# Optimization experiments

Measured on AMD Instinct MI355X. Metric: run time of the kernel, lower is better.

## Reference

```python
import jax, jax.numpy as jnp
import numpy as np

D_TEMP = 64   # temporal_dim (even)
H = 4         # num_heads
KQ = 128      # kq_dim = temporal_dim + sum(cat_dims)
LD = 128      # output_latent_dim == value_dim
NREF = 128    # num_ref_points
MINT, MAXT = 0.0, 1.0


def time_emb(t):
    # sinusoidal embedding, cont_model='sinusoidal', learn_emb=False
    # z[..., 0::2] = sin(48*t * div), z[..., 1::2] = cos(48*t * div)
    pos = 48.0 * t[..., None]
    div = jnp.exp(jnp.arange(0, D_TEMP, 2, dtype=jnp.float32) * (-np.log(10.0) / D_TEMP))
    ang = pos * div
    return jnp.stack([jnp.sin(ang), jnp.cos(ang)], axis=-1).reshape(*t.shape, D_TEMP)


def setup_inputs() -> dict:
    key = jax.random.key(0)
    ks = jax.random.split(key, 10)
    N, T = 4, 1024
    ts = jax.random.uniform(ks[0], (N, T), jnp.float32)
    ys0 = jax.random.randint(ks[1], (N, T), 0, 100)
    ys1 = jax.random.randint(ks[2], (N, T), 0, 50)
    x = jax.random.normal(ks[3], (N, T, LD), jnp.float32)
    s = lambda k, sh: jax.random.normal(k, sh, jnp.float32) * 0.02
    emb0 = s(ks[4], (101, 32))   # class_sizes[0]+1 rows; last row = null/query class
    emb1 = s(ks[5], (51, 32))
    Wq = s(ks[6], (KQ, H * KQ)); bq = jnp.zeros((H * KQ,), jnp.float32)
    Wk = s(ks[7], (KQ, H * KQ)); bk = jnp.zeros((H * KQ,), jnp.float32)
    Wo = s(ks[8], (H * LD, LD)); bo = jnp.zeros((LD,), jnp.float32)
    return dict(ts=ts, ys0=ys0, ys1=ys1, x=x, emb0=emb0, emb1=emb1,
                Wq=Wq, bq=bq, Wk=Wk, bk=bk, Wo=Wo, bo=bo)


def reference(ts, ys0, ys1, x, emb0, emb1, Wq, bq, Wk, bk, Wo, bo):
    N, T = ts.shape
    # keys: time embedding || class embeddings at observed times  [N,T,KQ]
    zys = jnp.concatenate([emb0[ys0], emb1[ys1]], axis=-1)
    k_in = jnp.concatenate([time_emb(ts), zys], axis=-1)
    # queries: time embedding of reference points || null-class embedding [N,NREF,KQ]
    ref = jnp.linspace(MINT, MAXT, NREF, dtype=jnp.float32)
    q_null = jnp.concatenate([emb0[100], emb1[50]])  # extra embedding row
    q_in = jnp.concatenate([time_emb(ref), jnp.broadcast_to(q_null, (NREF, q_null.shape[0]))], axis=-1)
    q_in = jnp.broadcast_to(q_in[None], (N, NREF, KQ))
    # multi-head attention (math identical to the broadcast/elementwise original)
    hq = (q_in @ Wq + bq).reshape(N, NREF, H, KQ)
    hk = (k_in @ Wk + bk).reshape(N, T, H, KQ)
    scores = jnp.einsum('bqhd,bkhd->bhqk', hq, hk) / np.sqrt(KQ)
    p = jax.nn.softmax(scores, axis=-1)
    # value shared across heads: sum_k p * v  == matmul
    out = jnp.einsum('bhqk,bkv->bqhv', p, x).reshape(N, NREF, H * LD)
    return out @ Wo + bo  # [N, NREF, LD]
```

## Files before the change

### kernel.cpp

```cpp
#include <hip/hip_runtime.h>
#include <hip/hip_bf16.h>

#define N_B   4
#define T_LEN 1024
#define NREF  128
#define H     4
#define KQ    128
#define LD    128
#define HKQ   512
#define HLD   512

typedef __attribute__((ext_vector_type(8))) short bf16x8;
typedef __attribute__((ext_vector_type(4))) float f32x4;

union V8 { __hip_bfloat16 h[8]; bf16x8 v; };
union V4 { __hip_bfloat16 h[4]; ushort4 u; };

__device__ __forceinline__ void sincos_pair(float t, int i, float* s, float* c) {
    float div = __expf(-(float)(2 * i) * (2.302585093f / 64.0f));
    __sincosf(48.0f * t * div, s, c);
}

__global__ __launch_bounds__(256) void pack_kernel(
    const float* __restrict__ ts, const int* __restrict__ ys0, const int* __restrict__ ys1,
    const float* __restrict__ x,
    const float* __restrict__ emb0, const float* __restrict__ emb1,
    const float* __restrict__ Wq, const float* __restrict__ bq,
    const float* __restrict__ Wk, const float* __restrict__ Wo,
    const float* __restrict__ bo,
    __hip_bfloat16* __restrict__ A, __hip_bfloat16* __restrict__ kin,
    __hip_bfloat16* __restrict__ xT, __hip_bfloat16* __restrict__ WoT,
    float* __restrict__ out)
{
    __shared__ __align__(16) unsigned char smem[49152];
    int job = blockIdx.x;
    int tid = threadIdx.x;

    if (job < 8) {
        __hip_bfloat16* buf0 = (__hip_bfloat16*)smem;
        __hip_bfloat16* wlds = (__hip_bfloat16*)(smem + 16384);
        int h = job >> 1, qbase = (job & 1) * 64;

        for (int u = 0; u < 4; ++u) {
            int slot = u * 256 + tid;
            int q = slot >> 4;
            int c0 = (slot & 15) * 8;
            V8 v;
            if (c0 < 64) {
                float t = (float)(qbase + q) / 127.0f;
                #pragma unroll
                for (int jj = 0; jj < 8; jj += 2) {
                    float s, c;
                    sincos_pair(t, (c0 + jj) >> 1, &s, &c);
                    v.h[jj] = __float2bfloat16(s);
                    v.h[jj + 1] = __float2bfloat16(c);
                }
            } else if (c0 < 96) {
                #pragma unroll
                for (int jj = 0; jj < 8; ++jj) v.h[jj] = __float2bfloat16(emb0[100 * 32 + (c0 - 64) + jj]);
            } else {
                #pragma unroll
                for (int jj = 0; jj < 8; ++jj) v.h[jj] = __float2bfloat16(emb1[50 * 32 + (c0 - 96) + jj]);
            }
            int idx = (q * 128 + c0) ^ ((q & 7) << 3);
            *(bf16x8*)&buf0[idx] = v.v;
        }
        for (int u = 0; u < 16; ++u) {
            int s = u * 256 + tid;
            int i = s >> 5;
            int d0 = (s & 31) * 4;
            float4 w = *(const float4*)&Wq[(size_t)i * HKQ + h * KQ + d0];
            float wv[4] = {w.x, w.y, w.z, w.w};
            #pragma unroll
            for (int jj = 0; jj < 4; ++jj) {
                int d = d0 + jj;
                wlds[(d * 128 + i) ^ ((d & 7) << 3)] = __float2bfloat16(wv[jj]);
            }
        }
        __syncthreads();

        int wave = tid >> 6, lane = tid & 63, lm = lane & 15, lg = lane >> 4;
        f32x4 acc[8];
        #pragma unroll
        for (int dt = 0; dt < 8; ++dt) acc[dt] = f32x4{0.f, 0.f, 0.f, 0.f};
        #pragma unroll
        for (int ks = 0; ks < 4; ++ks) {
            int q = wave * 16 + lm;
            bf16x8 af = *(bf16x8*)&buf0[(q * 128 + ks * 32 + 8 * lg) ^ ((q & 7) << 3)];
            #pragma unroll
            for (int dt = 0; dt < 8; ++dt) {
                int d = dt * 16 + lm;
                bf16x8 bfr = *(bf16x8*)&wlds[(d * 128 + ks * 32 + 8 * lg) ^ ((d & 7) << 3)];
                acc[dt] = __builtin_amdgcn_mfma_f32_16x16x32_bf16(af, bfr, acc[dt], 0, 0, 0);
            }
        }
        __syncthreads();
        #pragma unroll
        for (int dt = 0; dt < 8; ++dt) {
            int d = dt * 16 + lm;
            float bb = bq[h * KQ + d];
            #pragma unroll
            for (int r = 0; r < 4; ++r) {
                int q = wave * 16 + 4 * lg + r;
                buf0[(q * 128 + d) ^ ((q & 7) << 3)] = __float2bfloat16(acc[dt][r] + bb);
            }
        }
        for (int u = 0; u < 16; ++u) {
            int s = u * 256 + tid;
            int i = s >> 5;
            int d0 = (s & 31) * 4;
            float4 w = *(const float4*)&Wk[(size_t)i * HKQ + h * KQ + d0];
            V4 bv;
            bv.h[0] = __float2bfloat16(w.x); bv.h[1] = __float2bfloat16(w.y);
            bv.h[2] = __float2bfloat16(w.z); bv.h[3] = __float2bfloat16(w.w);
            *(ushort4*)&wlds[(i * 128 + d0) ^ ((i & 7) << 3)] = bv.u;
        }
        __syncthreads();
        f32x4 acc2[8];
        #pragma unroll
        for (int it = 0; it < 8; ++it) acc2[it] = f32x4{0.f, 0.f, 0.f, 0.f};
        #pragma unroll
        for (int ks = 0; ks < 4; ++ks) {
            int q = wave * 16 + lm;
            bf16x8 af = *(bf16x8*)&buf0[(q * 128 + ks * 32 + 8 * lg) ^ ((q & 7) << 3)];
            #pragma unroll
            for (int it = 0; it < 8; ++it) {
                int i2 = it * 16 + lm;
                bf16x8 bv = *(bf16x8*)&wlds[(i2 * 128 + ks * 32 + 8 * lg) ^ ((i2 & 7) << 3)];
                acc2[it] = __builtin_amdgcn_mfma_f32_16x16x32_bf16(af, bv, acc2[it], 0, 0, 0);
            }
        }
        #pragma unroll
        for (int it = 0; it < 8; ++it) {
            int i2 = it * 16 + lm;
            #pragma unroll
            for (int r = 0; r < 4; ++r) {
                int q = qbase + wave * 16 + 4 * lg + r;
                A[((size_t)h * NREF + q) * KQ + i2] = __float2bfloat16(acc2[it][r]);
            }
        }
    } else if (job < 72) {
        int row0 = (job - 8) * 64;
        for (int u = 0; u < 4; ++u) {
            int slot = u * 256 + tid;
            int r = slot >> 4;
            int c0 = (slot & 15) * 8;
            int bt = row0 + r;
            V8 v;
            if (c0 < 64) {
                float t = ts[bt];
                #pragma unroll
                for (int jj = 0; jj < 8; jj += 2) {
                    float s, c;
                    sincos_pair(t, (c0 + jj) >> 1, &s, &c);
                    v.h[jj] = __float2bfloat16(s);
                    v.h[jj + 1] = __float2bfloat16(c);
                }
            } else if (c0 < 96) {
                int y = ys0[bt];
                #pragma unroll
                for (int jj = 0; jj < 8; ++jj) v.h[jj] = __float2bfloat16(emb0[y * 32 + (c0 - 64) + jj]);
            } else {
                int y = ys1[bt];
                #pragma unroll
                for (int jj = 0; jj < 8; ++jj) v.h[jj] = __float2bfloat16(emb1[y * 32 + (c0 - 96) + jj]);
            }
            *(bf16x8*)&kin[(size_t)bt * KQ + c0] = v.v;
        }
    } else if (job < 136) {
        __hip_bfloat16 (*tile)[136] = (__hip_bfloat16(*)[136])smem;
        int jb = job - 72;
        int b = jb >> 4, t0 = (jb & 15) * 64;
        for (int e = tid; e < 64 * 32; e += 256) {
            int tt = e >> 5, v4 = e & 31;
            float4 xv = *(const float4*)&x[((size_t)(b * T_LEN + t0 + tt)) * LD + v4 * 4];
            tile[tt][v4 * 4 + 0] = __float2bfloat16(xv.x);
            tile[tt][v4 * 4 + 1] = __float2bfloat16(xv.y);
            tile[tt][v4 * 4 + 2] = __float2bfloat16(xv.z);
            tile[tt][v4 * 4 + 3] = __float2bfloat16(xv.w);
        }
        __syncthreads();
        int v = tid >> 1, th = (tid & 1) * 32;
        for (int i = 0; i < 32; i += 4) {
            ushort4 u;
            u.x = *(unsigned short*)&tile[th + i + 0][v];
            u.y = *(unsigned short*)&tile[th + i + 1][v];
            u.z = *(unsigned short*)&tile[th + i + 2][v];
            u.w = *(unsigned short*)&tile[th + i + 3][v];
            *(ushort4*)&xT[((size_t)b * LD + v) * T_LEN + t0 + th + i] = u;
        }
    } else if (job < 144) {
        __hip_bfloat16 (*tile)[130] = (__hip_bfloat16(*)[130])smem;
        int i0 = (job - 136) * 64;
        for (int u = 0; u < 32; ++u) {
            int e = u * 256 + tid;
            int il = e >> 7, j = e & 127;
            tile[il][j] = __float2bfloat16(Wo[(size_t)(i0 + il) * LD + j]);
        }
        __syncthreads();
        for (int u = 0; u < 32; ++u) {
            int s = u * 256 + tid;
            int j = s >> 6, il = s & 63;
            WoT[(size_t)j * HLD + i0 + il] = tile[il][j];
        }
    } else {
        int b = job - 144;
        for (int e = tid; e < NREF * LD; e += 256)
            out[(size_t)b * NREF * LD + e] = bo[e & 127];
    }
}

__global__ __launch_bounds__(512) void attn_proj(const __hip_bfloat16* __restrict__ A,
                                                 const __hip_bfloat16* __restrict__ kin,
                                                 const __hip_bfloat16* __restrict__ xT,
                                                 const __hip_bfloat16* __restrict__ WoT,
                                                 float* __restrict__ out) {
    __shared__ __hip_bfloat16 P_lds[16 * 1024];
    __shared__ __hip_bfloat16 att_lds[16 * 128];
    __shared__ float redm[8][16], reds[8][16];

    int tid = threadIdx.x;
    int w = tid >> 6, lane = tid & 63;
    int lm = lane & 15, lg = lane >> 4;
    int q0 = blockIdx.x * 16, h = blockIdx.y, b = blockIdx.z;
    const float scale = 0.08838834764831845f;

    bf16x8 af[4];
    #pragma unroll
    for (int ks = 0; ks < 4; ++ks)
        af[ks] = *(const bf16x8*)(A + ((size_t)h * NREF + q0 + lm) * KQ + ks * 32 + lg * 8);

    f32x4 sacc[8];
    #pragma unroll
    for (int kt = 0; kt < 8; ++kt) sacc[kt] = f32x4{0.f, 0.f, 0.f, 0.f};
    #pragma unroll
    for (int ks = 0; ks < 4; ++ks) {
        #pragma unroll
        for (int kt = 0; kt < 8; ++kt) {
            bf16x8 bfr = *(const bf16x8*)(kin + (size_t)(b * T_LEN + w * 128 + kt * 16 + lm) * KQ + ks * 32 + lg * 8);
            sacc[kt] = __builtin_amdgcn_mfma_f32_16x16x32_bf16(af[ks], bfr, sacc[kt], 0, 0, 0);
        }
    }
    #pragma unroll
    for (int r = 0; r < 4; ++r) {
        float cm = sacc[0][r];
        #pragma unroll
        for (int kt = 1; kt < 8; ++kt) cm = fmaxf(cm, sacc[kt][r]);
        #pragma unroll
        for (int o = 8; o >= 1; o >>= 1) cm = fmaxf(cm, __shfl_xor(cm, o));
        if (lm == 0) redm[w][4 * lg + r] = cm;
    }
    __syncthreads();
    #pragma unroll
    for (int r = 0; r < 4; ++r) {
        int q = 4 * lg + r;
        float cm = redm[0][q];
        #pragma unroll
        for (int ww = 1; ww < 8; ++ww) cm = fmaxf(cm, redm[ww][q]);
        float fm = cm * scale;
        float sum = 0.f;
        #pragma unroll
        for (int kt = 0; kt < 8; ++kt) {
            float p = __expf(sacc[kt][r] * scale - fm);
            sum += p;
            int key = w * 128 + kt * 16 + lm;
            P_lds[(q * 1024 + key) ^ ((q & 7) << 3)] = __float2bfloat16(p);
        }
        #pragma unroll
        for (int o = 8; o >= 1; o >>= 1) sum += __shfl_xor(sum, o);
        if (lm == 0) reds[w][q] = sum;
    }
    __syncthreads();
    float l_[4];
    #pragma unroll
    for (int r = 0; r < 4; ++r) {
        int q = 4 * lg + r;
        float csum = reds[0][q];
        #pragma unroll
        for (int ww = 1; ww < 8; ++ww) csum += reds[ww][q];
        l_[r] = csum;
    }
    f32x4 oacc = f32x4{0.f, 0.f, 0.f, 0.f};
    const __hip_bfloat16* xb0 = xT + (size_t)(b * LD + w * 16 + lm) * T_LEN;
    #pragma unroll
    for (int ks2 = 0; ks2 < 32; ++ks2) {
        bf16x8 pa = *(bf16x8*)&P_lds[(lm * 1024 + ks2 * 32 + 8 * lg) ^ ((lm & 7) << 3)];
        bf16x8 xb = *(const bf16x8*)(xb0 + ks2 * 32 + lg * 8);
        oacc = __builtin_amdgcn_mfma_f32_16x16x32_bf16(pa, xb, oacc, 0, 0, 0);
    }
    #pragma unroll
    for (int r = 0; r < 4; ++r) {
        int q = 4 * lg + r;
        att_lds[(q * 128 + w * 16 + lm) ^ ((q & 7) << 3)] = __float2bfloat16(oacc[r] / l_[r]);
    }
    __syncthreads();
    f32x4 cacc = f32x4{0.f, 0.f, 0.f, 0.f};
    #pragma unroll
    for (int ks = 0; ks < 4; ++ks) {
        bf16x8 aa = *(bf16x8*)&att_lds[(lm * 128 + ks * 32 + 8 * lg) ^ ((lm & 7) << 3)];
        bf16x8 wb = *(const bf16x8*)(WoT + (size_t)(w * 16 + lm) * HLD + h * LD + ks * 32 + lg * 8);
        cacc = __builtin_amdgcn_mfma_f32_16x16x32_bf16(aa, wb, cacc, 0, 0, 0);
    }
    #pragma unroll
    for (int r = 0; r < 4; ++r) {
        int q = q0 + 4 * lg + r;
        atomicAdd(&out[((size_t)b * NREF + q) * LD + w * 16 + lm], cacc[r]);
    }
}

extern "C" void kernel_launch(void* const* d_in, const int* in_sizes, int n_in,
                              void* d_out, int out_size, void* d_ws, size_t ws_size,
                              hipStream_t stream) {
    const float* ts   = (const float*)d_in[0];
    const int*   ys0  = (const int*)d_in[1];
    const int*   ys1  = (const int*)d_in[2];
    const float* x    = (const float*)d_in[3];
    const float* emb0 = (const float*)d_in[4];
    const float* emb1 = (const float*)d_in[5];
    const float* Wq   = (const float*)d_in[6];
    const float* bq   = (const float*)d_in[7];
    const float* Wk   = (const float*)d_in[8];
    const float* Wo   = (const float*)d_in[10];
    const float* bo   = (const float*)d_in[11];
    float* out = (float*)d_out;

    __hip_bfloat16* bfws = (__hip_bfloat16*)d_ws;
    __hip_bfloat16* A   = bfws;
    __hip_bfloat16* kin = A + 65536;
    __hip_bfloat16* xT  = kin + 524288;
    __hip_bfloat16* WoT = xT + 524288;

    hipLaunchKernelGGL(pack_kernel, dim3(148), dim3(256), 0, stream,
                       ts, ys0, ys1, x, emb0, emb1, Wq, bq, Wk, Wo, bo, A, kin, xT, WoT, out);
    hipLaunchKernelGGL(attn_proj, dim3(8, 4, 4), dim3(512), 0, stream, A, kin, xT, WoT, out);
}
```

Measured before the change: 36.53 us.

## Fuse pack and attention kernels into one cooperative kernel with grid sync

Merges the packing kernel and the attention/projection kernel into a single cooperative launch of 128 blocks of 512 threads, separated by a grid-wide barrier. The packing jobs are re-partitioned onto 112 of the blocks at 512 threads each, which means fewer, larger blocks for the Q/K-projection prologue. This aims to remove the second kernel launch and the inter-kernel gap. In exchange it adds grid-sync overhead and cooperative-launch constraints, and the head-projection prologue now runs on only 4 blocks instead of 8, which lengthens that serial phase.

```diff
diff --git a/kernel.cpp b/kernel.cpp
--- a/kernel.cpp
+++ b/kernel.cpp
@@ -1,5 +1,8 @@
 #include <hip/hip_runtime.h>
 #include <hip/hip_bf16.h>
+#include <hip/hip_cooperative_groups.h>
+
+namespace cg = cooperative_groups;
 
 #define N_B   4
 #define T_LEN 1024
@@ -21,7 +24,7 @@
     __sincosf(48.0f * t * div, s, c);
 }
 
-__global__ __launch_bounds__(256) void pack_kernel(
+__global__ __launch_bounds__(512) void fused_all(
     const float* __restrict__ ts, const int* __restrict__ ys0, const int* __restrict__ ys1,
     const float* __restrict__ x,
     const float* __restrict__ emb0, const float* __restrict__ emb1,
@@ -32,22 +35,23 @@
     __hip_bfloat16* __restrict__ xT, __hip_bfloat16* __restrict__ WoT,
     float* __restrict__ out)
 {
-    __shared__ __align__(16) unsigned char smem[49152];
+    __shared__ __align__(16) unsigned char smem[65536];
+    int tid = threadIdx.x;
     int job = blockIdx.x;
-    int tid = threadIdx.x;
-
-    if (job < 8) {
+    const float scale = 0.08838834764831845f;
+
+    if (job < 4) {
         __hip_bfloat16* buf0 = (__hip_bfloat16*)smem;
-        __hip_bfloat16* wlds = (__hip_bfloat16*)(smem + 16384);
-        int h = job >> 1, qbase = (job & 1) * 64;
+        __hip_bfloat16* wlds = (__hip_bfloat16*)(smem + 32768);
+        int h = job;
 
         for (int u = 0; u < 4; ++u) {
-            int slot = u * 256 + tid;
+            int slot = u * 512 + tid;
             int q = slot >> 4;
             int c0 = (slot & 15) * 8;
             V8 v;
             if (c0 < 64) {
-                float t = (float)(qbase + q) / 127.0f;
+                float t = (float)q / 127.0f;
                 #pragma unroll
                 for (int jj = 0; jj < 8; jj += 2) {
                     float s, c;
@@ -65,8 +69,8 @@
             int idx = (q * 128 + c0) ^ ((q & 7) << 3);
             *(bf16x8*)&buf0[idx] = v.v;
         }
-        for (int u = 0; u < 16; ++u) {
-            int s = u * 256 + tid;
+        for (int u = 0; u < 8; ++u) {
+            int s = u * 512 + tid;
             int i = s >> 5;
             int d0 = (s & 31) * 4;
             float4 w = *(const float4*)&Wq[(size_t)i * HKQ + h * KQ + d0];
@@ -105,8 +109,8 @@
                 buf0[(q * 128 + d) ^ ((q & 7) << 3)] = __float2bfloat16(acc[dt][r] + bb);
             }
         }
-        for (int u = 0; u < 16; ++u) {
-            int s = u * 256 + tid;
+        for (int u = 0; u < 8; ++u) {
+            int s = u * 512 + tid;
             int i = s >> 5;
             int d0 = (s & 31) * 4;
             float4 w = *(const float4*)&Wk[(size_t)i * HKQ + h * KQ + d0];
@@ -135,14 +139,14 @@
             int i2 = it * 16 + lm;
             #pragma unroll
             for (int r = 0; r < 4; ++r) {
-                int q = qbase + wave * 16 + 4 * lg + r;
+                int q = wave * 16 + 4 * lg + r;
                 A[((size_t)h * NREF + q) * KQ + i2] = __float2bfloat16(acc2[it][r]);
             }
         }
-    } else if (job < 72) {
-        int row0 = (job - 8) * 64;
+    } else if (job < 36) {
+        int row0 = (job - 4) * 128;
         for (int u = 0; u < 4; ++u) {
-            int slot = u * 256 + tid;
+            int slot = u * 512 + tid;
             int r = slot >> 4;
             int c0 = (slot & 15) * 8;
             int bt = row0 + r;
@@ -167,11 +171,12 @@
             }
             *(bf16x8*)&kin[(size_t)bt * KQ + c0] = v.v;
         }
-    } else if (job < 136) {
+    } else if (job < 100) {
         __hip_bfloat16 (*tile)[136] = (__hip_bfloat16(*)[136])smem;
-        int jb = job - 72;
+        int jb = job - 36;
         int b = jb >> 4, t0 = (jb & 15) * 64;
-        for (int e = tid; e < 64 * 32; e += 256) {
+        for (int u = 0; u < 4; ++u) {
+            int e = u * 512 + tid;
             int tt = e >> 5, v4 = e & 31;
             float4 xv = *(const float4*)&x[((size_t)(b * T_LEN + t0 + tt)) * LD + v4 * 4];
             tile[tt][v4 * 4 + 0] = __float2bfloat16(xv.x);
@@ -180,8 +185,8 @@
             tile[tt][v4 * 4 + 3] = __float2bfloat16(xv.w);
         }
         __syncthreads();
-        int v = tid >> 1, th = (tid & 1) * 32;
-        for (int i = 0; i < 32; i += 4) {
+        int v = tid >> 2, th = (tid & 3) * 16;
+        for (int i = 0; i < 16; i += 4) {
             ushort4 u;
             u.x = *(unsigned short*)&tile[th + i + 0][v];
             u.y = *(unsigned short*)&tile[th + i + 1][v];
@@ -189,122 +194,121 @@
             u.w = *(unsigned short*)&tile[th + i + 3][v];
             *(ushort4*)&xT[((size_t)b * LD + v) * T_LEN + t0 + th + i] = u;
         }
-    } else if (job < 144) {
+    } else if (job < 108) {
         __hip_bfloat16 (*tile)[130] = (__hip_bfloat16(*)[130])smem;
-        int i0 = (job - 136) * 64;
-        for (int u = 0; u < 32; ++u) {
-            int e = u * 256 + tid;
+        int i0 = (job - 100) * 64;
+        for (int u = 0; u < 16; ++u) {
+            int e = u * 512 + tid;
             int il = e >> 7, j = e & 127;
             tile[il][j] = __float2bfloat16(Wo[(size_t)(i0 + il) * LD + j]);
         }
         __syncthreads();
-        for (int u = 0; u < 32; ++u) {
-            int s = u * 256 + tid;
+        for (int u = 0; u < 16; ++u) {
+            int s = u * 512 + tid;
             int j = s >> 6, il = s & 63;
             WoT[(size_t)j * HLD + i0 + il] = tile[il][j];
         }
-    } else {
-        int b = job - 144;
-        for (int e = tid; e < NREF * LD; e += 256)
+    } else if (job < 112) {
+        int b = job - 108;
+        for (int e = tid; e < NREF * LD; e += 512)
             out[(size_t)b * NREF * LD + e] = bo[e & 127];
     }
-}
-
-__global__ __launch_bounds__(512) void attn_proj(const __hip_bfloat16* __restrict__ A,
-                                                 const __hip_bfloat16* __restrict__ kin,
-                                                 const __hip_bfloat16* __restrict__ xT,
-                                                 const __hip_bfloat16* __restrict__ WoT,
-                                                 float* __restrict__ out) {
-    __shared__ __hip_bfloat16 P_lds[16 * 1024];
-    __shared__ __hip_bfloat16 att_lds[16 * 128];
-    __shared__ float redm[8][16], reds[8][16];
-
-    int tid = threadIdx.x;
-    int w = tid >> 6, lane = tid & 63;
-    int lm = lane & 15, lg = lane >> 4;
-    int q0 = blockIdx.x * 16, h = blockIdx.y, b = blockIdx.z;
-    const float scale = 0.08838834764831845f;
-
-    bf16x8 af[4];
-    #pragma unroll
-    for (int ks = 0; ks < 4; ++ks)
-        af[ks] = *(const bf16x8*)(A + ((size_t)h * NREF + q0 + lm) * KQ + ks * 32 + lg * 8);
-
-    f32x4 sacc[8];
-    #pragma unroll
-    for (int kt = 0; kt < 8; ++kt) sacc[kt] = f32x4{0.f, 0.f, 0.f, 0.f};
-    #pragma unroll
-    for (int ks = 0; ks < 4; ++ks) {
-        #pragma unroll
-        for (int kt = 0; kt < 8; ++kt) {
-            bf16x8 bfr = *(const bf16x8*)(kin + (size_t)(b * T_LEN + w * 128 + kt * 16 + lm) * KQ + ks * 32 + lg * 8);
-            sacc[kt] = __builtin_amdgcn_mfma_f32_16x16x32_bf16(af[ks], bfr, sacc[kt], 0, 0, 0);
-        }
-    }
-    #pragma unroll
-    for (int r = 0; r < 4; ++r) {
-        float cm = sacc[0][r];
-        #pragma unroll
-        for (int kt = 1; kt < 8; ++kt) cm = fmaxf(cm, sacc[kt][r]);
-        #pragma unroll
-        for (int o = 8; o >= 1; o >>= 1) cm = fmaxf(cm, __shfl_xor(cm, o));
-        if (lm == 0) redm[w][4 * lg + r] = cm;
-    }
-    __syncthreads();
-    #pragma unroll
-    for (int r = 0; r < 4; ++r) {
-        int q = 4 * lg + r;
-        float cm = redm[0][q];
-        #pragma unroll
-        for (int ww = 1; ww < 8; ++ww) cm = fmaxf(cm, redm[ww][q]);
-        float fm = cm * scale;
-        float sum = 0.f;
-        #pragma unroll
-        for (int kt = 0; kt < 8; ++kt) {
-            float p = __expf(sacc[kt][r] * scale - fm);
-            sum += p;
-            int key = w * 128 + kt * 16 + lm;
-            P_lds[(q * 1024 + key) ^ ((q & 7) << 3)] = __float2bfloat16(p);
-        }
-        #pragma unroll
-        for (int o = 8; o >= 1; o >>= 1) sum += __shfl_xor(sum, o);
-        if (lm == 0) reds[w][q] = sum;
-    }
-    __syncthreads();
-    float l_[4];
-    #pragma unroll
-    for (int r = 0; r < 4; ++r) {
-        int q = 4 * lg + r;
-        float csum = reds[0][q];
-        #pragma unroll
-        for (int ww = 1; ww < 8; ++ww) csum += reds[ww][q];
-        l_[r] = csum;
-    }
-    f32x4 oacc = f32x4{0.f, 0.f, 0.f, 0.f};
-    const __hip_bfloat16* xb0 = xT + (size_t)(b * LD + w * 16 + lm) * T_LEN;
-    #pragma unroll
-    for (int ks2 = 0; ks2 < 32; ++ks2) {
-        bf16x8 pa = *(bf16x8*)&P_lds[(lm * 1024 + ks2 * 32 + 8 * lg) ^ ((lm & 7) << 3)];
-        bf16x8 xb = *(const bf16x8*)(xb0 + ks2 * 32 + lg * 8);
-        oacc = __builtin_amdgcn_mfma_f32_16x16x32_bf16(pa, xb, oacc, 0, 0, 0);
-    }
-    #pragma unroll
-    for (int r = 0; r < 4; ++r) {
-        int q = 4 * lg + r;
-        att_lds[(q * 128 + w * 16 + lm) ^ ((q & 7) << 3)] = __float2bfloat16(oacc[r] / l_[r]);
-    }
-    __syncthreads();
-    f32x4 cacc = f32x4{0.f, 0.f, 0.f, 0.f};
-    #pragma unroll
-    for (int ks = 0; ks < 4; ++ks) {
-        bf16x8 aa = *(bf16x8*)&att_lds[(lm * 128 + ks * 32 + 8 * lg) ^ ((lm & 7) << 3)];
-        bf16x8 wb = *(const bf16x8*)(WoT + (size_t)(w * 16 + lm) * HLD + h * LD + ks * 32 + lg * 8);
-        cacc = __builtin_amdgcn_mfma_f32_16x16x32_bf16(aa, wb, cacc, 0, 0, 0);
-    }
-    #pragma unroll
-    for (int r = 0; r < 4; ++r) {
-        int q = q0 + 4 * lg + r;
-        atomicAdd(&out[((size_t)b * NREF + q) * LD + w * 16 + lm], cacc[r]);
+
+    cg::this_grid().sync();
+
+    {
+        __hip_bfloat16* P_lds   = (__hip_bfloat16*)smem;
+        __hip_bfloat16* att_lds = (__hip_bfloat16*)(smem + 32768);
+        float* redm = (float*)(smem + 36864);
+        float* reds = (float*)(smem + 37376);
+
+        int w = tid >> 6, lane = tid & 63;
+        int lm = lane & 15, lg = lane >> 4;
+        int blk = blockIdx.x;
+        int qt = blk & 7, h = (blk >> 3) & 3, b = blk >> 5;
+        int q0 = qt * 16;
+
+        bf16x8 af[4];
+        #pragma unroll
+        for (int ks = 0; ks < 4; ++ks)
+            af[ks] = *(const bf16x8*)(A + ((size_t)h * NREF + q0 + lm) * KQ + ks * 32 + lg * 8);
+
+        f32x4 sacc[8];
+        #pragma unroll
+        for (int kt = 0; kt < 8; ++kt) sacc[kt] = f32x4{0.f, 0.f, 0.f, 0.f};
+        #pragma unroll
+        for (int ks = 0; ks < 4; ++ks) {
+            #pragma unroll
+            for (int kt = 0; kt < 8; ++kt) {
+                bf16x8 bfr = *(const bf16x8*)(kin + (size_t)(b * T_LEN + w * 128 + kt * 16 + lm) * KQ + ks * 32 + lg * 8);
+                sacc[kt] = __builtin_amdgcn_mfma_f32_16x16x32_bf16(af[ks], bfr, sacc[kt], 0, 0, 0);
+            }
+        }
+        #pragma unroll
+        for (int r = 0; r < 4; ++r) {
+            float cm = sacc[0][r];
+            #pragma unroll
+            for (int kt = 1; kt < 8; ++kt) cm = fmaxf(cm, sacc[kt][r]);
+            #pragma unroll
+            for (int o = 8; o >= 1; o >>= 1) cm = fmaxf(cm, __shfl_xor(cm, o));
+            if (lm == 0) redm[w * 16 + 4 * lg + r] = cm;
+        }
+        __syncthreads();
+        #pragma unroll
+        for (int r = 0; r < 4; ++r) {
+            int q = 4 * lg + r;
+            float cm = redm[q];
+            #pragma unroll
+            for (int ww = 1; ww < 8; ++ww) cm = fmaxf(cm, redm[ww * 16 + q]);
+            float fm = cm * scale;
+            float sum = 0.f;
+            #pragma unroll
+            for (int kt = 0; kt < 8; ++kt) {
+                float p = __expf(sacc[kt][r] * scale - fm);
+                sum += p;
+                int key = w * 128 + kt * 16 + lm;
+                P_lds[(q * 1024 + key) ^ ((q & 7) << 3)] = __float2bfloat16(p);
+            }
+            #pragma unroll
+            for (int o = 8; o >= 1; o >>= 1) sum += __shfl_xor(sum, o);
+            if (lm == 0) reds[w * 16 + q] = sum;
+        }
+        __syncthreads();
+        float l_[4];
+        #pragma unroll
+        for (int r = 0; r < 4; ++r) {
+            int q = 4 * lg + r;
+            float csum = reds[q];
+            #pragma unroll
+            for (int ww = 1; ww < 8; ++ww) csum += reds[ww * 16 + q];
+            l_[r] = csum;
+        }
+        f32x4 oacc = f32x4{0.f, 0.f, 0.f, 0.f};
+        const __hip_bfloat16* xb0 = xT + (size_t)(b * LD + w * 16 + lm) * T_LEN;
+        #pragma unroll
+        for (int ks2 = 0; ks2 < 32; ++ks2) {
+            bf16x8 pa = *(bf16x8*)&P_lds[(lm * 1024 + ks2 * 32 + 8 * lg) ^ ((lm & 7) << 3)];
+            bf16x8 xb = *(const bf16x8*)(xb0 + ks2 * 32 + lg * 8);
+            oacc = __builtin_amdgcn_mfma_f32_16x16x32_bf16(pa, xb, oacc, 0, 0, 0);
+        }
+        #pragma unroll
+        for (int r = 0; r < 4; ++r) {
+            int q = 4 * lg + r;
+            att_lds[(q * 128 + w * 16 + lm) ^ ((q & 7) << 3)] = __float2bfloat16(oacc[r] / l_[r]);
+        }
+        __syncthreads();
+        f32x4 cacc = f32x4{0.f, 0.f, 0.f, 0.f};
+        #pragma unroll
+        for (int ks = 0; ks < 4; ++ks) {
+            bf16x8 aa = *(bf16x8*)&att_lds[(lm * 128 + ks * 32 + 8 * lg) ^ ((lm & 7) << 3)];
+            bf16x8 wb = *(const bf16x8*)(WoT + (size_t)(w * 16 + lm) * HLD + h * LD + ks * 32 + lg * 8);
+            cacc = __builtin_amdgcn_mfma_f32_16x16x32_bf16(aa, wb, cacc, 0, 0, 0);
+        }
+        #pragma unroll
+        for (int r = 0; r < 4; ++r) {
+            int q = q0 + 4 * lg + r;
+            atomicAdd(&out[((size_t)b * NREF + q) * LD + w * 16 + lm], cacc[r]);
+        }
     }
 }
 
@@ -330,7 +334,11 @@
     __hip_bfloat16* xT  = kin + 524288;
     __hip_bfloat16* WoT = xT + 524288;
 
-    hipLaunchKernelGGL(pack_kernel, dim3(148), dim3(256), 0, stream,
-                       ts, ys0, ys1, x, emb0, emb1, Wq, bq, Wk, Wo, bo, A, kin, xT, WoT, out);
-    hipLaunchKernelGGL(attn_proj, dim3(8, 4, 4), dim3(512), 0, stream, A, kin, xT, WoT, out);
+    void* args[] = {
+        (void*)&ts, (void*)&ys0, (void*)&ys1, (void*)&x,
+        (void*)&emb0, (void*)&emb1, (void*)&Wq, (void*)&bq,
+        (void*)&Wk, (void*)&Wo, (void*)&bo,
+        (void*)&A, (void*)&kin, (void*)&xT, (void*)&WoT, (void*)&out
+    };
+    hipLaunchCooperativeKernel((const void*)fused_all, dim3(128), dim3(512), args, 0, stream);
 }
```

Result: slower. 65.58 us (+79.5%).

## Split attention over key chunks with atomic partials and last-block output projection

Applied to the files above, without the earlier changes.

Splits the key dimension of the attention kernel into two 512-key chunks, doubling the grid to 256 blocks. Unnormalised numerators and denominators are accumulated with float atomics into a workspace, and the softmax max-subtraction is dropped. A per-query-tile counter picks the last arriving block, which normalises, runs the full 512-wide Wo projection, and writes the output with bias directly. This removes the output atomics and the bias-init pass. In exchange it adds workspace zeroing, atomic traffic, threadfence synchronisation, and a risk of exp overflow without the max shift.

```diff
diff --git a/kernel.cpp b/kernel.cpp
--- a/kernel.cpp
+++ b/kernel.cpp
@@ -16,6 +16,8 @@
 union V8 { __hip_bfloat16 h[8]; bf16x8 v; };
 union V4 { __hip_bfloat16 h[4]; ushort4 u; };
 
+#define MFMA(a, b, c) __builtin_amdgcn_mfma_f32_16x16x32_bf16((a), (b), (c), 0, 0, 0)
+
 __device__ __forceinline__ void sincos_pair(float t, int i, float* s, float* c) {
     float div = __expf(-(float)(2 * i) * (2.302585093f / 64.0f));
     __sincosf(48.0f * t * div, s, c);
@@ -27,10 +29,9 @@
     const float* __restrict__ emb0, const float* __restrict__ emb1,
     const float* __restrict__ Wq, const float* __restrict__ bq,
     const float* __restrict__ Wk, const float* __restrict__ Wo,
-    const float* __restrict__ bo,
     __hip_bfloat16* __restrict__ A, __hip_bfloat16* __restrict__ kin,
     __hip_bfloat16* __restrict__ xT, __hip_bfloat16* __restrict__ WoT,
-    float* __restrict__ out)
+    float* __restrict__ Nws, float* __restrict__ Dws, unsigned int* __restrict__ counters)
 {
     __shared__ __align__(16) unsigned char smem[49152];
     int job = blockIdx.x;
@@ -91,7 +92,7 @@
             for (int dt = 0; dt < 8; ++dt) {
                 int d = dt * 16 + lm;
                 bf16x8 bfr = *(bf16x8*)&wlds[(d * 128 + ks * 32 + 8 * lg) ^ ((d & 7) << 3)];
-                acc[dt] = __builtin_amdgcn_mfma_f32_16x16x32_bf16(af, bfr, acc[dt], 0, 0, 0);
+                acc[dt] = MFMA(af, bfr, acc[dt]);
             }
         }
         __syncthreads();
@@ -127,7 +128,7 @@
             for (int it = 0; it < 8; ++it) {
                 int i2 = it * 16 + lm;
                 bf16x8 bv = *(bf16x8*)&wlds[(i2 * 128 + ks * 32 + 8 * lg) ^ ((i2 & 7) << 3)];
-                acc2[it] = __builtin_amdgcn_mfma_f32_16x16x32_bf16(af, bv, acc2[it], 0, 0, 0);
+                acc2[it] = MFMA(af, bv, acc2[it]);
             }
         }
         #pragma unroll
@@ -204,25 +205,32 @@
             WoT[(size_t)j * HLD + i0 + il] = tile[il][j];
         }
     } else {
-        int b = job - 144;
-        for (int e = tid; e < NREF * LD; e += 256)
-            out[(size_t)b * NREF * LD + e] = bo[e & 127];
+        int z = job - 144;
+        float4 zz = make_float4(0.f, 0.f, 0.f, 0.f);
+        float* base = Nws + (size_t)z * 32768;
+        for (int e = tid; e < 8192; e += 256) *(float4*)&base[e * 4] = zz;
+        if (z == 0) {
+            for (int e = tid; e < 2048; e += 256) Dws[e] = 0.f;
+            if (tid < 32) counters[tid] = 0u;
+        }
     }
 }
 
-__global__ __launch_bounds__(512) void attn_proj(const __hip_bfloat16* __restrict__ A,
-                                                 const __hip_bfloat16* __restrict__ kin,
-                                                 const __hip_bfloat16* __restrict__ xT,
-                                                 const __hip_bfloat16* __restrict__ WoT,
-                                                 float* __restrict__ out) {
-    __shared__ __hip_bfloat16 P_lds[16 * 1024];
-    __shared__ __hip_bfloat16 att_lds[16 * 128];
-    __shared__ float redm[8][16], reds[8][16];
+__global__ __launch_bounds__(512) void attnz(const __hip_bfloat16* __restrict__ A,
+                                             const __hip_bfloat16* __restrict__ kin,
+                                             const __hip_bfloat16* __restrict__ xT,
+                                             const __hip_bfloat16* __restrict__ WoT,
+                                             const float* __restrict__ bo,
+                                             float* Nws, float* Dws,
+                                             unsigned int* counters, float* out) {
+    __shared__ __hip_bfloat16 P_lds[16 * 512];
+    __shared__ int flagv;
 
     int tid = threadIdx.x;
     int w = tid >> 6, lane = tid & 63;
     int lm = lane & 15, lg = lane >> 4;
-    int q0 = blockIdx.x * 16, h = blockIdx.y, b = blockIdx.z;
+    int qt = blockIdx.x, h = blockIdx.y & 3, tc = blockIdx.y >> 2, b = blockIdx.z;
+    int q0 = qt * 16;
     const float scale = 0.08838834764831845f;
 
     bf16x8 af[4];
@@ -230,81 +238,79 @@
     for (int ks = 0; ks < 4; ++ks)
         af[ks] = *(const bf16x8*)(A + ((size_t)h * NREF + q0 + lm) * KQ + ks * 32 + lg * 8);
 
-    f32x4 sacc[8];
-    #pragma unroll
-    for (int kt = 0; kt < 8; ++kt) sacc[kt] = f32x4{0.f, 0.f, 0.f, 0.f};
+    f32x4 sacc[4];
+    #pragma unroll
+    for (int kt = 0; kt < 4; ++kt) sacc[kt] = f32x4{0.f, 0.f, 0.f, 0.f};
+    int kbase = b * T_LEN + tc * 512 + w * 64;
     #pragma unroll
     for (int ks = 0; ks < 4; ++ks) {
         #pragma unroll
-        for (int kt = 0; kt < 8; ++kt) {
-            bf16x8 bfr = *(const bf16x8*)(kin + (size_t)(b * T_LEN + w * 128 + kt * 16 + lm) * KQ + ks * 32 + lg * 8);
-            sacc[kt] = __builtin_amdgcn_mfma_f32_16x16x32_bf16(af[ks], bfr, sacc[kt], 0, 0, 0);
-        }
-    }
-    #pragma unroll
-    for (int r = 0; r < 4; ++r) {
-        float cm = sacc[0][r];
-        #pragma unroll
-        for (int kt = 1; kt < 8; ++kt) cm = fmaxf(cm, sacc[kt][r]);
-        #pragma unroll
-        for (int o = 8; o >= 1; o >>= 1) cm = fmaxf(cm, __shfl_xor(cm, o));
-        if (lm == 0) redm[w][4 * lg + r] = cm;
-    }
-    __syncthreads();
+        for (int kt = 0; kt < 4; ++kt) {
+            bf16x8 bfr = *(const bf16x8*)(kin + (size_t)(kbase + kt * 16 + lm) * KQ + ks * 32 + lg * 8);
+            sacc[kt] = MFMA(af[ks], bfr, sacc[kt]);
+        }
+    }
     #pragma unroll
     for (int r = 0; r < 4; ++r) {
         int q = 4 * lg + r;
-        float cm = redm[0][q];
-        #pragma unroll
-        for (int ww = 1; ww < 8; ++ww) cm = fmaxf(cm, redm[ww][q]);
-        float fm = cm * scale;
         float sum = 0.f;
         #pragma unroll
-        for (int kt = 0; kt < 8; ++kt) {
-            float p = __expf(sacc[kt][r] * scale - fm);
+        for (int kt = 0; kt < 4; ++kt) {
+            float p = __expf(sacc[kt][r] * scale);
             sum += p;
-            int key = w * 128 + kt * 16 + lm;
-            P_lds[(q * 1024 + key) ^ ((q & 7) << 3)] = __float2bfloat16(p);
+            int key = w * 64 + kt * 16 + lm;
+            P_lds[(q * 512 + key) ^ ((q & 7) << 3)] = __float2bfloat16(p);
         }
         #pragma unroll
         for (int o = 8; o >= 1; o >>= 1) sum += __shfl_xor(sum, o);
-        if (lm == 0) reds[w][q] = sum;
+        if (lm == 0) atomicAdd(&Dws[((size_t)b * H + h) * NREF + q0 + q], sum);
     }
     __syncthreads();
-    float l_[4];
-    #pragma unroll
-    for (int r = 0; r < 4; ++r) {
-        int q = 4 * lg + r;
-        float csum = reds[0][q];
-        #pragma unroll
-        for (int ww = 1; ww < 8; ++ww) csum += reds[ww][q];
-        l_[r] = csum;
-    }
+
     f32x4 oacc = f32x4{0.f, 0.f, 0.f, 0.f};
-    const __hip_bfloat16* xb0 = xT + (size_t)(b * LD + w * 16 + lm) * T_LEN;
-    #pragma unroll
-    for (int ks2 = 0; ks2 < 32; ++ks2) {
-        bf16x8 pa = *(bf16x8*)&P_lds[(lm * 1024 + ks2 * 32 + 8 * lg) ^ ((lm & 7) << 3)];
+    const __hip_bfloat16* xb0 = xT + (size_t)(b * LD + w * 16 + lm) * T_LEN + tc * 512;
+    #pragma unroll
+    for (int ks2 = 0; ks2 < 16; ++ks2) {
+        bf16x8 pa = *(bf16x8*)&P_lds[(lm * 512 + ks2 * 32 + lg * 8) ^ ((lm & 7) << 3)];
         bf16x8 xb = *(const bf16x8*)(xb0 + ks2 * 32 + lg * 8);
-        oacc = __builtin_amdgcn_mfma_f32_16x16x32_bf16(pa, xb, oacc, 0, 0, 0);
-    }
-    #pragma unroll
-    for (int r = 0; r < 4; ++r) {
-        int q = 4 * lg + r;
-        att_lds[(q * 128 + w * 16 + lm) ^ ((q & 7) << 3)] = __float2bfloat16(oacc[r] / l_[r]);
-    }
-    __syncthreads();
-    f32x4 cacc = f32x4{0.f, 0.f, 0.f, 0.f};
-    #pragma unroll
-    for (int ks = 0; ks < 4; ++ks) {
-        bf16x8 aa = *(bf16x8*)&att_lds[(lm * 128 + ks * 32 + 8 * lg) ^ ((lm & 7) << 3)];
-        bf16x8 wb = *(const bf16x8*)(WoT + (size_t)(w * 16 + lm) * HLD + h * LD + ks * 32 + lg * 8);
-        cacc = __builtin_amdgcn_mfma_f32_16x16x32_bf16(aa, wb, cacc, 0, 0, 0);
+        oacc = MFMA(pa, xb, oacc);
     }
     #pragma unroll
     for (int r = 0; r < 4; ++r) {
         int q = q0 + 4 * lg + r;
-        atomicAdd(&out[((size_t)b * NREF + q) * LD + w * 16 + lm], cacc[r]);
+        atomicAdd(&Nws[((size_t)b * NREF + q) * HLD + h * LD + w * 16 + lm], oacc[r]);
+    }
+
+    __threadfence();
+    __syncthreads();
+    if (tid == 0) {
+        unsigned int old = atomicAdd(&counters[b * 8 + qt], 1u);
+        flagv = ((old & 7u) == 7u) ? 1 : 0;
+    }
+    __syncthreads();
+    if (!flagv) return;
+    __threadfence();
+
+    for (int e = tid; e < 16 * 512; e += 512) {
+        int q = e >> 9, hv = e & 511, hh = hv >> 7;
+        float d = Dws[((size_t)b * H + hh) * NREF + q0 + q];
+        float n = Nws[((size_t)b * NREF + q0 + q) * HLD + hv];
+        P_lds[(q * 512 + hv) ^ ((q & 7) << 3)] = __float2bfloat16(n / d);
+    }
+    __syncthreads();
+
+    f32x4 cacc = f32x4{0.f, 0.f, 0.f, 0.f};
+    #pragma unroll
+    for (int ks = 0; ks < 16; ++ks) {
+        bf16x8 aa = *(bf16x8*)&P_lds[(lm * 512 + ks * 32 + lg * 8) ^ ((lm & 7) << 3)];
+        bf16x8 wb = *(const bf16x8*)(WoT + (size_t)(w * 16 + lm) * HLD + ks * 32 + lg * 8);
+        cacc = MFMA(aa, wb, cacc);
+    }
+    float bb = bo[w * 16 + lm];
+    #pragma unroll
+    for (int r = 0; r < 4; ++r) {
+        int q = q0 + 4 * lg + r;
+        out[((size_t)b * NREF + q) * LD + w * 16 + lm] = cacc[r] + bb;
     }
 }
 
@@ -329,8 +335,13 @@
     __hip_bfloat16* kin = A + 65536;
     __hip_bfloat16* xT  = kin + 524288;
     __hip_bfloat16* WoT = xT + 524288;
-
-    hipLaunchKernelGGL(pack_kernel, dim3(148), dim3(256), 0, stream,
-                       ts, ys0, ys1, x, emb0, emb1, Wq, bq, Wk, Wo, bo, A, kin, xT, WoT, out);
-    hipLaunchKernelGGL(attn_proj, dim3(8, 4, 4), dim3(512), 0, stream, A, kin, xT, WoT, out);
+    float* Nws = (float*)((char*)d_ws + 2359296);
+    float* Dws = Nws + 262144;
+    unsigned int* counters = (unsigned int*)(Dws + 2048);
+
+    hipLaunchKernelGGL(pack_kernel, dim3(152), dim3(256), 0, stream,
+                       ts, ys0, ys1, x, emb0, emb1, Wq, bq, Wk, Wo,
+                       A, kin, xT, WoT, Nws, Dws, counters);
+    hipLaunchKernelGGL(attnz, dim3(8, 8, 4), dim3(512), 0, stream,
+                       A, kin, xT, WoT, bo, Nws, Dws, counters, out);
 }
```

New measurement: 69.07 us. +89.1%, slower.
